# Kernel optimization log

Measured on AMD Instinct MI355X. Metric: run time of the kernel, lower is better.

Reference implementation:

```python
import jax, jax.numpy as jnp
import numpy as np

EPS = 1e-06

def setup_inputs() -> dict:
    key = jax.random.key(0)
    kx, kq, kk, kv = jax.random.split(key, 4)
    B, S, D, F = 8, 4096, 1024, 1024
    # glorot-uniform-ish scale for weights
    scale = (6.0 / (D + F)) ** 0.5
    x = jax.random.normal(kx, (B, S, D), dtype=jnp.float32)
    Wq = jax.random.uniform(kq, (D, F), dtype=jnp.float32, minval=-scale, maxval=scale)
    Wk = jax.random.uniform(kk, (D, F), dtype=jnp.float32, minval=-scale, maxval=scale)
    Wv = jax.random.uniform(kv, (D, F), dtype=jnp.float32, minval=-scale, maxval=scale)
    return {"x": x, "Wq": Wq, "Wk": Wk, "Wv": Wv}


def reference(x, Wq, Wk, Wv):
    # x: [B, S, D]; projections -> [B, S, F]
    queries = jnp.einsum('bsd,df->bsf', x, Wq)
    keys = jnp.einsum('bsd,df->bsf', x, Wk)
    values = jnp.einsum('bsd,df->bsf', x, Wv)
    # feature map: relu(.) + 1 (strictly positive kernel features)
    queries = jax.nn.relu(queries) + 1.0
    keys = jax.nn.relu(keys) + 1.0
    # numerator: K^T V over sequence -> [B, F, F]
    numerator = jnp.einsum('bsf,bsg->bfg', keys, values)
    # denominator: sum of keys over sequence -> [B, 1, F]; broadcasts over last axis
    denominator = jnp.sum(keys, axis=-2, keepdims=True)
    context = numerator / (denominator + EPS)
    # output: context @ Q^T -> [B, F, S]
    output = jnp.einsum('bfg,bsg->bfs', context, queries)
    return output
```

## Files before the change

### kernel.cpp

```cpp
#include <hip/hip_runtime.h>


#define EPSF 1e-6f

constexpr int Bb = 8;
constexpr int Ss = 4096;
constexpr int Dd = 1024;
constexpr int Ff = 1024;

typedef __attribute__((ext_vector_type(8))) short   bf16x8;
typedef __attribute__((ext_vector_type(8))) unsigned short u16x8;
typedef __attribute__((ext_vector_type(4))) float   f32x4;

typedef __attribute__((address_space(3))) unsigned char lds_u8;
typedef __attribute__((address_space(3))) const bf16x8  lds_cvec;

static __device__ __forceinline__ unsigned short f2bf(float f) {
    union { float f; unsigned int u; } v; v.f = f;
    unsigned int r = (v.u + 0x7fffu + ((v.u >> 16) & 1u)) >> 16;
    return (unsigned short)r;
}
static __device__ __forceinline__ float bf2f(unsigned short u) {
    union { unsigned int u; float f; } v; v.u = ((unsigned int)u) << 16;
    return v.f;
}

static __device__ __forceinline__ void gld_lds16(const void* g, lds_u8* l) {
    __builtin_amdgcn_global_load_lds(
        (const __attribute__((address_space(1))) unsigned int*)g,
        (__attribute__((address_space(3))) unsigned int*)l,
        16, 0, 0);
}

__global__ void cvt_x_kernel(const float* __restrict__ x, unsigned short* __restrict__ xb, int n4)
{
    int i = blockIdx.x * blockDim.x + threadIdx.x;
    if (i >= n4) return;
    float4 v = *(const float4*)&x[(size_t)i * 4];
    ushort4 o;
    o.x = f2bf(v.x); o.y = f2bf(v.y); o.z = f2bf(v.z); o.w = f2bf(v.w);
    *(ushort4*)&xb[(size_t)i * 4] = o;
}

__global__ void cvt_wT_kernel(const float* __restrict__ Wq,
                              const float* __restrict__ Wk,
                              const float* __restrict__ Wv,
                              unsigned short* __restrict__ WT)
{
    const int z = blockIdx.z;
    const float* __restrict__ W = (z == 0) ? Wq : (z == 1 ? Wk : Wv);
    unsigned short* __restrict__ dst = WT + (size_t)z * Dd * Ff;

    __shared__ float tile[32][33];
    const int tid = threadIdx.x;
    const int d0 = blockIdx.y * 32, f0 = blockIdx.x * 32;
    const int c = tid & 31, r8 = tid >> 5;
#pragma unroll
    for (int p = 0; p < 4; ++p) {
        int r = p * 8 + r8;
        tile[r][c] = W[(size_t)(d0 + r) * Ff + f0 + c];
    }
    __syncthreads();
#pragma unroll
    for (int p = 0; p < 4; ++p) {
        int r = p * 8 + r8;
        dst[(size_t)(f0 + r) * Dd + d0 + c] = f2bf(tile[c][r]);
    }
}

__global__ void den_kernel(const unsigned short* __restrict__ KbT, float* __restrict__ den)
{
    const int tid = threadIdx.x;
    const int w = tid >> 6, lane = tid & 63;
    const int f = blockIdx.x * 4 + w;
    const int b = blockIdx.y;
    const unsigned short* __restrict__ row = KbT + ((size_t)b * Ff + f) * Ss;
    float s = 0.f;
#pragma unroll
    for (int it = 0; it < Ss / 512; ++it) {
        u16x8 v = *(const u16x8*)&row[it * 512 + lane * 8];
#pragma unroll
        for (int j = 0; j < 8; ++j) s += bf2f(v[j]);
    }
#pragma unroll
    for (int off = 32; off > 0; off >>= 1) s += __shfl_down(s, off, 64);
    if (lane == 0) den[(size_t)b * Ff + f] = s;
}

__global__ void add_ctx_kernel(const unsigned short* __restrict__ p,
                               unsigned short* __restrict__ c)
{
    const int b = blockIdx.y;
    const size_t i8 = ((size_t)blockIdx.x * 256 + threadIdx.x) * 8;
    const u16x8 a0 = *(const u16x8*)(p + (size_t)(2 * b) * Ff * Ff + i8);
    const u16x8 a1 = *(const u16x8*)(p + (size_t)(2 * b + 1) * Ff * Ff + i8);
    u16x8 o;
#pragma unroll
    for (int j = 0; j < 8; ++j) o[j] = f2bf(bf2f(a0[j]) + bf2f(a1[j]));
    *(u16x8*)(c + (size_t)b * Ff * Ff + i8) = o;
}

template<int ACT, int SCALE, int OUT_BF16, int SPLITK2>
__global__ __launch_bounds__(512, 2)
void gemm8(const unsigned short* __restrict__ A,
           const unsigned short* __restrict__ Bt,
           void* __restrict__ Cout,
           const float* __restrict__ den,
           int lda, int ldb, int ldc, int Kdim,
           size_t strideA, size_t strideB, size_t strideC)
{
    __shared__ __align__(16) unsigned char smem_[131072];
    lds_u8* const smem = (lds_u8*)smem_;

    const int gx = gridDim.x, gxy = gx * gridDim.y;
    int flat = blockIdx.z * gxy + blockIdx.y * gx + blockIdx.x;
    const int nwg = gxy * gridDim.z;
    const int cpx = nwg >> 3;
    flat = (flat & 7) * cpx + (flat >> 3);
    const int z = flat / gxy;
    const int rem = flat - z * gxy;
    const int by = rem / gx;
    const int bx = rem - by * gx;

    const int zb   = SPLITK2 ? (z >> 1) : z;
    const int koff = SPLITK2 ? ((z & 1) * Kdim) : 0;

    const unsigned short* __restrict__ Ag  = A  + strideA * zb + koff;
    const unsigned short* __restrict__ Bg  = Bt + strideB * zb + koff;
    const float* __restrict__ denb = SCALE ? (den + (size_t)zb * Ff) : nullptr;

    const int bm = by * 256;
    const int bn = bx * 256;

    const int tid  = threadIdx.x;
    const int wv   = tid >> 6, lane = tid & 63;
    const int wm   = wv >> 2, wn = wv & 3;
    const int lm   = lane & 15;
    const int kg16 = (lane >> 4) << 4;
    const int swz  = (lm & 7) << 4;
    const int kbs  = (((tid & 7) ^ ((tid >> 3) & 7)) << 4);
    const int srow = tid >> 3;

    f32x4 acc[8][4];
#pragma unroll
    for (int i = 0; i < 8; ++i)
#pragma unroll
        for (int j = 0; j < 4; ++j) acc[i][j] = (f32x4){0.f, 0.f, 0.f, 0.f};

    lds_u8* const A0 = smem;
    lds_u8* const B0 = smem + 32768;
    lds_u8* const A1 = smem + 65536;
    lds_u8* const B1 = smem + 98304;

    auto STAGE = [&](int ts, int m, int buf, int h) {
        const unsigned short* gb = m ? Bg : Ag;
        const int ld = m ? ldb : lda;
        const int off0 = m ? bn : bm;
        lds_u8* lb = smem + buf * 65536 + m * 32768 + h * 16384 + wv * 1024;
#pragma unroll
        for (int q = 0; q < 2; ++q) {
            int row = h * 128 + q * 64 + srow;
            const unsigned char* g =
                (const unsigned char*)(gb + (size_t)(off0 + row) * ld + ts * 64) + kbs;
            gld_lds16(g, lb + q * 8192);
        }
    };
    auto LDA4 = [&](bf16x8* dst, int fmb, int kk, lds_u8* Ab) {
#pragma unroll
        for (int f = 0; f < 4; ++f) {
            int r = wm * 128 + (fmb + f) * 16 + lm;
            dst[f] = *(lds_cvec*)(Ab + r * 128 + ((kk * 64 + kg16) ^ swz));
        }
    };
    auto LDB4 = [&](bf16x8* dst, int kk, lds_u8* Bb) {
#pragma unroll
        for (int f = 0; f < 4; ++f) {
            int c = wn * 64 + f * 16 + lm;
            dst[f] = *(lds_cvec*)(Bb + c * 128 + ((kk * 64 + kg16) ^ swz));
        }
    };

#define MM16(a4, b4, mo)                                                        \
    do {                                                                        \
        __builtin_amdgcn_s_setprio(1);                                          \
        _Pragma("unroll")                                                       \
        for (int fm = 0; fm < 4; ++fm)                                          \
            _Pragma("unroll")                                                   \
            for (int fn = 0; fn < 4; ++fn)                                      \
                acc[(mo) + fm][fn] = __builtin_amdgcn_mfma_f32_16x16x32_bf16(   \
                    (b4)[fn], (a4)[fm], acc[(mo) + fm][fn], 0, 0, 0);           \
        __builtin_amdgcn_s_setprio(0);                                          \
    } while (0)

#define FENCE_IN()                                                  \
    do {                                                            \
        __builtin_amdgcn_s_barrier();                               \
        asm volatile("s_waitcnt lgkmcnt(0)");                       \
    } while (0)
#define BAR() __builtin_amdgcn_s_barrier()
#define VM4() asm volatile("s_waitcnt vmcnt(4)")

    const int NT = Kdim >> 6;
    const int NI = NT >> 1;

    STAGE(0, 1, 0, 0); STAGE(0, 1, 0, 1);
    STAGE(0, 0, 0, 0); STAGE(0, 0, 0, 1);
    STAGE(1, 1, 1, 0); STAGE(1, 1, 1, 1);
    VM4();
    BAR();

    for (int i = 0; i < NI; ++i) {
        const int t = 2 * i;
        const int t1s = t + 1;
        const int t2s = (t + 2 < NT) ? t + 2 : NT - 1;
        const int t3s = (t + 3 < NT) ? t + 3 : NT - 1;

        bf16x8 b0r[4], b1r[4], a0r[4], a1r[4];
        LDB4(b0r, 0, B0); LDA4(a0r, 0, 0, A0);
        STAGE(t1s, 0, 1, 0);
        FENCE_IN(); MM16(a0r, b0r, 0); BAR();
        LDA4(a1r, 4, 0, A0); LDB4(b1r, 1, B0);
        STAGE(t1s, 0, 1, 1);
        FENCE_IN(); MM16(a1r, b0r, 4); BAR();
        LDA4(a0r, 0, 1, A0);
        STAGE(t2s, 1, 0, 0);
        FENCE_IN(); MM16(a0r, b1r, 0); BAR();
        LDA4(a1r, 4, 1, A0);
        STAGE(t2s, 1, 0, 1);
        FENCE_IN(); MM16(a1r, b1r, 4); VM4(); BAR();
        LDB4(b0r, 0, B1); LDA4(a0r, 0, 0, A1);
        STAGE(t2s, 0, 0, 0);
        FENCE_IN(); MM16(a0r, b0r, 0); BAR();
        LDA4(a1r, 4, 0, A1); LDB4(b1r, 1, B1);
        STAGE(t2s, 0, 0, 1);
        FENCE_IN(); MM16(a1r, b0r, 4); BAR();
        LDA4(a0r, 0, 1, A1);
        STAGE(t3s, 1, 1, 0);
        FENCE_IN(); MM16(a0r, b1r, 0); BAR();
        LDA4(a1r, 4, 1, A1);
        STAGE(t3s, 1, 1, 1);
        FENCE_IN(); MM16(a1r, b1r, 4); VM4(); BAR();
    }

    asm volatile("s_waitcnt vmcnt(0)");

    const int hi4 = (lane >> 4) * 4;
#pragma unroll
    for (int fm = 0; fm < 8; ++fm) {
        const int gr = bm + wm * 128 + fm * 16 + lm;
#pragma unroll
        for (int fn = 0; fn < 4; ++fn) {
            const int gcn = bn + wn * 64 + fn * 16 + hi4;
            f32x4 v = acc[fm][fn];
            if (ACT) {
#pragma unroll
                for (int e = 0; e < 4; ++e) v[e] = fmaxf(v[e], 0.f) + 1.f;
            }
            if (SCALE) {
                float4 d4 = *(const float4*)&denb[gcn];
                v[0] *= 1.f / (d4.x + EPSF);
                v[1] *= 1.f / (d4.y + EPSF);
                v[2] *= 1.f / (d4.z + EPSF);
                v[3] *= 1.f / (d4.w + EPSF);
            }
            if (OUT_BF16) {
                ushort4 o;
                o.x = f2bf(v[0]); o.y = f2bf(v[1]); o.z = f2bf(v[2]); o.w = f2bf(v[3]);
                *(ushort4*)((unsigned short*)Cout + strideC * z + (size_t)gr * ldc + gcn) = o;
            } else {
                *(float4*)((float*)Cout + strideC * z + (size_t)gr * ldc + gcn) =
                    *(float4*)&v;
            }
        }
    }
#undef MM16
#undef FENCE_IN
#undef BAR
#undef VM4
}

extern "C" void kernel_launch(void* const* d_in, const int* in_sizes, int n_in,
                              void* d_out, int out_size, void* d_ws, size_t ws_size,
                              hipStream_t stream)
{
    (void)in_sizes; (void)n_in; (void)out_size;
    const float* x  = (const float*)d_in[0];
    const float* Wq = (const float*)d_in[1];
    const float* Wk = (const float*)d_in[2];
    const float* Wv = (const float*)d_in[3];
    float* out = (float*)d_out;

    const size_t nx   = (size_t)Bb * Ss * Dd;
    const size_t nW   = (size_t)3 * Dd * Ff;
    const size_t nQKV = (size_t)Bb * Ss * Ff;
    const size_t nCtx = (size_t)Bb * Ff * Ff;
    const size_t nP   = (size_t)16 * Ff * Ff;

    unsigned short* xb   = (unsigned short*)d_ws;
    unsigned short* WT   = xb + nx;
    unsigned short* Qb   = WT + nW;
    unsigned short* KbT  = Qb + nQKV;
    unsigned short* VbT  = KbT + nQKV;
    unsigned short* ctxb = VbT + nQKV;
    float* den = (float*)(ctxb + nCtx);
    unsigned short* pctx = (unsigned short*)(den + (size_t)Bb * Ff);

    const size_t need_split =
        ((nx + nW + 3 * nQKV + nCtx + nP) * 2 + (size_t)Bb * Ff * 4);
    const bool do_split = ws_size >= need_split;

    cvt_x_kernel<<<dim3((int)(nx / 4 / 256)), 256, 0, stream>>>(x, xb, (int)(nx / 4));
    cvt_wT_kernel<<<dim3(Ff / 32, Dd / 32, 3), 256, 0, stream>>>(Wq, Wk, Wv, WT);

    gemm8<1, 0, 1, 0><<<dim3(Ss / 256, Ff / 256, Bb), 512, 0, stream>>>(
        WT + (size_t)1 * Dd * Ff, xb, KbT, nullptr,
        Dd, Dd, Ss, Dd, 0, (size_t)Ss * Dd, (size_t)Ff * Ss);

    den_kernel<<<dim3(Ff / 4, Bb), 256, 0, stream>>>(KbT, den);

    gemm8<1, 1, 1, 0><<<dim3(Ff / 256, Ss / 256, Bb), 512, 0, stream>>>(
        xb, WT + (size_t)0 * Dd * Ff, Qb, den,
        Dd, Dd, Ff, Dd, (size_t)Ss * Dd, 0, (size_t)Ss * Ff);

    gemm8<0, 0, 1, 0><<<dim3(Ss / 256, Ff / 256, Bb), 512, 0, stream>>>(
        WT + (size_t)2 * Dd * Ff, xb, VbT, nullptr,
        Dd, Dd, Ss, Dd, 0, (size_t)Ss * Dd, (size_t)Ff * Ss);

    if (do_split) {
        gemm8<0, 0, 1, 1><<<dim3(Ff / 256, Ff / 256, 2 * Bb), 512, 0, stream>>>(
            KbT, VbT, pctx, nullptr,
            Ss, Ss, Ff, Ss / 2, (size_t)Ff * Ss, (size_t)Ff * Ss, (size_t)Ff * Ff);
        add_ctx_kernel<<<dim3(Ff * Ff / 8 / 256, Bb), 256, 0, stream>>>(pctx, ctxb);
    } else {
        gemm8<0, 0, 1, 0><<<dim3(Ff / 256, Ff / 256, Bb), 512, 0, stream>>>(
            KbT, VbT, ctxb, nullptr,
            Ss, Ss, Ff, Ss, (size_t)Ff * Ss, (size_t)Ff * Ss, (size_t)Ff * Ff);
    }

    gemm8<0, 0, 0, 0><<<dim3(Ss / 256, Ff / 256, Bb), 512, 0, stream>>>(
        ctxb, Qb, out, nullptr,
        Ff, Ff, Ss, Ff, (size_t)Ff * Ff, (size_t)Ss * Ff, (size_t)Ff * Ss);
}
```

Baseline: 414.0 us.

## Software-pipeline LDS fragment loads one phase ahead of MFMA in GEMM loop

```diff
diff --git a/kernel.cpp b/kernel.cpp
--- a/kernel.cpp
+++ b/kernel.cpp
@@ -192,13 +192,18 @@
         __builtin_amdgcn_s_setprio(0);                                          \
     } while (0)
 
-#define FENCE_IN()                                                  \
+#define PHEND()                                                     \
     do {                                                            \
+        asm volatile("s_waitcnt lgkmcnt(0)");                       \
+        __builtin_amdgcn_sched_barrier(0);                          \
         __builtin_amdgcn_s_barrier();                               \
-        asm volatile("s_waitcnt lgkmcnt(0)");                       \
     } while (0)
-#define BAR() __builtin_amdgcn_s_barrier()
-#define VM4() asm volatile("s_waitcnt vmcnt(4)")
+#define PHEND_VM2()                                                 \
+    do {                                                            \
+        asm volatile("s_waitcnt vmcnt(2) lgkmcnt(0)");              \
+        __builtin_amdgcn_sched_barrier(0);                          \
+        __builtin_amdgcn_s_barrier();                               \
+    } while (0)
 
     const int NT = Kdim >> 6;
     const int NI = NT >> 1;
@@ -206,8 +211,11 @@
     STAGE(0, 1, 0, 0); STAGE(0, 1, 0, 1);
     STAGE(0, 0, 0, 0); STAGE(0, 0, 0, 1);
     STAGE(1, 1, 1, 0); STAGE(1, 1, 1, 1);
-    VM4();
-    BAR();
+    asm volatile("s_waitcnt vmcnt(4)");
+    __builtin_amdgcn_s_barrier();
+
+    bf16x8 a03[4], a47[4], b0[4], b1[4];
+    LDB4(b0, 0, B0); LDA4(a03, 0, 0, A0);
 
     for (int i = 0; i < NI; ++i) {
         const int t = 2 * i;
@@ -215,31 +223,38 @@
         const int t2s = (t + 2 < NT) ? t + 2 : NT - 1;
         const int t3s = (t + 3 < NT) ? t + 3 : NT - 1;
 
-        bf16x8 b0r[4], b1r[4], a0r[4], a1r[4];
-        LDB4(b0r, 0, B0); LDA4(a0r, 0, 0, A0);
         STAGE(t1s, 0, 1, 0);
-        FENCE_IN(); MM16(a0r, b0r, 0); BAR();
-        LDA4(a1r, 4, 0, A0); LDB4(b1r, 1, B0);
+        LDA4(a47, 4, 0, A0);
+        MM16(a03, b0, 0);
+        PHEND();
         STAGE(t1s, 0, 1, 1);
-        FENCE_IN(); MM16(a1r, b0r, 4); BAR();
-        LDA4(a0r, 0, 1, A0);
+        LDA4(a03, 0, 1, A0); LDB4(b1, 1, B0);
+        MM16(a47, b0, 4);
+        PHEND();
         STAGE(t2s, 1, 0, 0);
-        FENCE_IN(); MM16(a0r, b1r, 0); BAR();
-        LDA4(a1r, 4, 1, A0);
+        LDA4(a47, 4, 1, A0);
+        MM16(a03, b1, 0);
+        PHEND_VM2();
         STAGE(t2s, 1, 0, 1);
-        FENCE_IN(); MM16(a1r, b1r, 4); VM4(); BAR();
-        LDB4(b0r, 0, B1); LDA4(a0r, 0, 0, A1);
+        LDA4(a03, 0, 0, A1); LDB4(b0, 0, B1);
+        MM16(a47, b1, 4);
+        PHEND();
         STAGE(t2s, 0, 0, 0);
-        FENCE_IN(); MM16(a0r, b0r, 0); BAR();
-        LDA4(a1r, 4, 0, A1); LDB4(b1r, 1, B1);
+        LDA4(a47, 4, 0, A1);
+        MM16(a03, b0, 0);
+        PHEND();
         STAGE(t2s, 0, 0, 1);
-        FENCE_IN(); MM16(a1r, b0r, 4); BAR();
-        LDA4(a0r, 0, 1, A1);
+        LDA4(a03, 0, 1, A1); LDB4(b1, 1, B1);
+        MM16(a47, b0, 4);
+        PHEND();
         STAGE(t3s, 1, 1, 0);
-        FENCE_IN(); MM16(a0r, b1r, 0); BAR();
-        LDA4(a1r, 4, 1, A1);
+        LDA4(a47, 4, 1, A1);
+        MM16(a03, b1, 0);
+        PHEND_VM2();
         STAGE(t3s, 1, 1, 1);
-        FENCE_IN(); MM16(a1r, b1r, 4); VM4(); BAR();
+        LDA4(a03, 0, 0, A0); LDB4(b0, 0, B0);
+        MM16(a47, b1, 4);
+        PHEND();
     }
 
     asm volatile("s_waitcnt vmcnt(0)");
@@ -274,9 +289,8 @@
         }
     }
 #undef MM16
-#undef FENCE_IN
-#undef BAR
-#undef VM4
+#undef PHEND
+#undef PHEND_VM2
 }
 
 extern "C" void kernel_launch(void* const* d_in, const int* in_sizes, int n_in,
```

After: 412.7 us. About the same (-0.3%).

## Shrink GEMM tiles to 128x128 with 4 waves and simple double-buffered loop

Applied to the files above, without the earlier changes.

```diff
diff --git a/kernel.cpp b/kernel.cpp
--- a/kernel.cpp
+++ b/kernel.cpp
@@ -101,7 +101,7 @@
 }
 
 template<int ACT, int SCALE, int OUT_BF16, int SPLITK2>
-__global__ __launch_bounds__(512, 2)
+__global__ __launch_bounds__(256, 2)
 void gemm8(const unsigned short* __restrict__ A,
            const unsigned short* __restrict__ Bt,
            void* __restrict__ Cout,
@@ -109,7 +109,7 @@
            int lda, int ldb, int ldc, int Kdim,
            size_t strideA, size_t strideB, size_t strideC)
 {
-    __shared__ __align__(16) unsigned char smem_[131072];
+    __shared__ __align__(16) unsigned char smem_[65536];
     lds_u8* const smem = (lds_u8*)smem_;
 
     const int gx = gridDim.x, gxy = gx * gridDim.y;
@@ -129,125 +129,93 @@
     const unsigned short* __restrict__ Bg  = Bt + strideB * zb + koff;
     const float* __restrict__ denb = SCALE ? (den + (size_t)zb * Ff) : nullptr;
 
-    const int bm = by * 256;
-    const int bn = bx * 256;
+    const int bm = by * 128;
+    const int bn = bx * 128;
 
     const int tid  = threadIdx.x;
     const int wv   = tid >> 6, lane = tid & 63;
-    const int wm   = wv >> 2, wn = wv & 3;
+    const int wm   = wv >> 1, wn = wv & 1;
     const int lm   = lane & 15;
     const int kg16 = (lane >> 4) << 4;
     const int swz  = (lm & 7) << 4;
     const int kbs  = (((tid & 7) ^ ((tid >> 3) & 7)) << 4);
     const int srow = tid >> 3;
 
-    f32x4 acc[8][4];
-#pragma unroll
-    for (int i = 0; i < 8; ++i)
+    f32x4 acc[4][4];
+#pragma unroll
+    for (int i = 0; i < 4; ++i)
 #pragma unroll
         for (int j = 0; j < 4; ++j) acc[i][j] = (f32x4){0.f, 0.f, 0.f, 0.f};
 
-    lds_u8* const A0 = smem;
-    lds_u8* const B0 = smem + 32768;
-    lds_u8* const A1 = smem + 65536;
-    lds_u8* const B1 = smem + 98304;
-
-    auto STAGE = [&](int ts, int m, int buf, int h) {
+    auto STAGE = [&](int ts, int m, int buf) {
         const unsigned short* gb = m ? Bg : Ag;
         const int ld = m ? ldb : lda;
         const int off0 = m ? bn : bm;
-        lds_u8* lb = smem + buf * 65536 + m * 32768 + h * 16384 + wv * 1024;
-#pragma unroll
-        for (int q = 0; q < 2; ++q) {
-            int row = h * 128 + q * 64 + srow;
+        lds_u8* lb = smem + buf * 32768 + m * 16384 + wv * 1024;
+#pragma unroll
+        for (int q = 0; q < 4; ++q) {
+            int row = q * 32 + srow;
             const unsigned char* g =
                 (const unsigned char*)(gb + (size_t)(off0 + row) * ld + ts * 64) + kbs;
-            gld_lds16(g, lb + q * 8192);
+            gld_lds16(g, lb + q * 4096);
         }
     };
-    auto LDA4 = [&](bf16x8* dst, int fmb, int kk, lds_u8* Ab) {
+    auto LD4 = [&](bf16x8* dst, int kk, lds_u8* base, int w0) {
 #pragma unroll
         for (int f = 0; f < 4; ++f) {
-            int r = wm * 128 + (fmb + f) * 16 + lm;
-            dst[f] = *(lds_cvec*)(Ab + r * 128 + ((kk * 64 + kg16) ^ swz));
+            int r = w0 * 64 + f * 16 + lm;
+            dst[f] = *(lds_cvec*)(base + r * 128 + ((kk * 64 + kg16) ^ swz));
         }
     };
-    auto LDB4 = [&](bf16x8* dst, int kk, lds_u8* Bb) {
-#pragma unroll
-        for (int f = 0; f < 4; ++f) {
-            int c = wn * 64 + f * 16 + lm;
-            dst[f] = *(lds_cvec*)(Bb + c * 128 + ((kk * 64 + kg16) ^ swz));
-        }
-    };
-
-#define MM16(a4, b4, mo)                                                        \
+
+#define MM16(a4, b4)                                                            \
     do {                                                                        \
         __builtin_amdgcn_s_setprio(1);                                          \
         _Pragma("unroll")                                                       \
         for (int fm = 0; fm < 4; ++fm)                                          \
             _Pragma("unroll")                                                   \
             for (int fn = 0; fn < 4; ++fn)                                      \
-                acc[(mo) + fm][fn] = __builtin_amdgcn_mfma_f32_16x16x32_bf16(   \
-                    (b4)[fn], (a4)[fm], acc[(mo) + fm][fn], 0, 0, 0);           \
+                acc[fm][fn] = __builtin_amdgcn_mfma_f32_16x16x32_bf16(          \
+                    (b4)[fn], (a4)[fm], acc[fm][fn], 0, 0, 0);                  \
         __builtin_amdgcn_s_setprio(0);                                          \
     } while (0)
 
-#define FENCE_IN()                                                  \
+#define LGKM0_FENCE()                                               \
     do {                                                            \
-        __builtin_amdgcn_s_barrier();                               \
         asm volatile("s_waitcnt lgkmcnt(0)");                       \
+        __builtin_amdgcn_sched_barrier(0);                          \
     } while (0)
-#define BAR() __builtin_amdgcn_s_barrier()
-#define VM4() asm volatile("s_waitcnt vmcnt(4)")
 
     const int NT = Kdim >> 6;
-    const int NI = NT >> 1;
-
-    STAGE(0, 1, 0, 0); STAGE(0, 1, 0, 1);
-    STAGE(0, 0, 0, 0); STAGE(0, 0, 0, 1);
-    STAGE(1, 1, 1, 0); STAGE(1, 1, 1, 1);
-    VM4();
-    BAR();
-
-    for (int i = 0; i < NI; ++i) {
-        const int t = 2 * i;
-        const int t1s = t + 1;
-        const int t2s = (t + 2 < NT) ? t + 2 : NT - 1;
-        const int t3s = (t + 3 < NT) ? t + 3 : NT - 1;
-
-        bf16x8 b0r[4], b1r[4], a0r[4], a1r[4];
-        LDB4(b0r, 0, B0); LDA4(a0r, 0, 0, A0);
-        STAGE(t1s, 0, 1, 0);
-        FENCE_IN(); MM16(a0r, b0r, 0); BAR();
-        LDA4(a1r, 4, 0, A0); LDB4(b1r, 1, B0);
-        STAGE(t1s, 0, 1, 1);
-        FENCE_IN(); MM16(a1r, b0r, 4); BAR();
-        LDA4(a0r, 0, 1, A0);
-        STAGE(t2s, 1, 0, 0);
-        FENCE_IN(); MM16(a0r, b1r, 0); BAR();
-        LDA4(a1r, 4, 1, A0);
-        STAGE(t2s, 1, 0, 1);
-        FENCE_IN(); MM16(a1r, b1r, 4); VM4(); BAR();
-        LDB4(b0r, 0, B1); LDA4(a0r, 0, 0, A1);
-        STAGE(t2s, 0, 0, 0);
-        FENCE_IN(); MM16(a0r, b0r, 0); BAR();
-        LDA4(a1r, 4, 0, A1); LDB4(b1r, 1, B1);
-        STAGE(t2s, 0, 0, 1);
-        FENCE_IN(); MM16(a1r, b0r, 4); BAR();
-        LDA4(a0r, 0, 1, A1);
-        STAGE(t3s, 1, 1, 0);
-        FENCE_IN(); MM16(a0r, b1r, 0); BAR();
-        LDA4(a1r, 4, 1, A1);
-        STAGE(t3s, 1, 1, 1);
-        FENCE_IN(); MM16(a1r, b1r, 4); VM4(); BAR();
-    }
-
+
+    STAGE(0, 0, 0); STAGE(0, 1, 0);
     asm volatile("s_waitcnt vmcnt(0)");
+    __builtin_amdgcn_s_barrier();
+
+    for (int t = 0; t < NT; ++t) {
+        const int buf = t & 1;
+        lds_u8* Ab  = smem + buf * 32768;
+        lds_u8* Bbs = Ab + 16384;
+        if (t + 1 < NT) {
+            STAGE(t + 1, 0, buf ^ 1);
+            STAGE(t + 1, 1, buf ^ 1);
+        }
+        bf16x8 a0[4], b0r[4], a1[4], b1r[4];
+        LD4(a0, 0, Ab, wm); LD4(b0r, 0, Bbs, wn);
+        LGKM0_FENCE();
+        MM16(a0, b0r);
+        LD4(a1, 1, Ab, wm); LD4(b1r, 1, Bbs, wn);
+        LGKM0_FENCE();
+        MM16(a1, b1r);
+        asm volatile("s_waitcnt vmcnt(0)");
+        __builtin_amdgcn_sched_barrier(0);
+        __builtin_amdgcn_s_barrier();
+    }
 
     const int hi4 = (lane >> 4) * 4;
 #pragma unroll
-    for (int fm = 0; fm < 8; ++fm) {
-        const int gr = bm + wm * 128 + fm * 16 + lm;
+    for (int fm = 0; fm < 4; ++fm) {
+        const int gr = bm + wm * 64 + fm * 16 + lm;
 #pragma unroll
         for (int fn = 0; fn < 4; ++fn) {
             const int gcn = bn + wn * 64 + fn * 16 + hi4;
@@ -274,9 +242,7 @@
         }
     }
 #undef MM16
-#undef FENCE_IN
-#undef BAR
-#undef VM4
+#undef LGKM0_FENCE
 }
 
 extern "C" void kernel_launch(void* const* d_in, const int* in_sizes, int n_in,
@@ -312,32 +278,32 @@
     cvt_x_kernel<<<dim3((int)(nx / 4 / 256)), 256, 0, stream>>>(x, xb, (int)(nx / 4));
     cvt_wT_kernel<<<dim3(Ff / 32, Dd / 32, 3), 256, 0, stream>>>(Wq, Wk, Wv, WT);
 
-    gemm8<1, 0, 1, 0><<<dim3(Ss / 256, Ff / 256, Bb), 512, 0, stream>>>(
+    gemm8<1, 0, 1, 0><<<dim3(Ss / 128, Ff / 128, Bb), 256, 0, stream>>>(
         WT + (size_t)1 * Dd * Ff, xb, KbT, nullptr,
         Dd, Dd, Ss, Dd, 0, (size_t)Ss * Dd, (size_t)Ff * Ss);
 
     den_kernel<<<dim3(Ff / 4, Bb), 256, 0, stream>>>(KbT, den);
 
-    gemm8<1, 1, 1, 0><<<dim3(Ff / 256, Ss / 256, Bb), 512, 0, stream>>>(
+    gemm8<1, 1, 1, 0><<<dim3(Ff / 128, Ss / 128, Bb), 256, 0, stream>>>(
         xb, WT + (size_t)0 * Dd * Ff, Qb, den,
         Dd, Dd, Ff, Dd, (size_t)Ss * Dd, 0, (size_t)Ss * Ff);
 
-    gemm8<0, 0, 1, 0><<<dim3(Ss / 256, Ff / 256, Bb), 512, 0, stream>>>(
+    gemm8<0, 0, 1, 0><<<dim3(Ss / 128, Ff / 128, Bb), 256, 0, stream>>>(
         WT + (size_t)2 * Dd * Ff, xb, VbT, nullptr,
         Dd, Dd, Ss, Dd, 0, (size_t)Ss * Dd, (size_t)Ff * Ss);
 
     if (do_split) {
-        gemm8<0, 0, 1, 1><<<dim3(Ff / 256, Ff / 256, 2 * Bb), 512, 0, stream>>>(
+        gemm8<0, 0, 1, 1><<<dim3(Ff / 128, Ff / 128, 2 * Bb), 256, 0, stream>>>(
             KbT, VbT, pctx, nullptr,
             Ss, Ss, Ff, Ss / 2, (size_t)Ff * Ss, (size_t)Ff * Ss, (size_t)Ff * Ff);
         add_ctx_kernel<<<dim3(Ff * Ff / 8 / 256, Bb), 256, 0, stream>>>(pctx, ctxb);
     } else {
-        gemm8<0, 0, 1, 0><<<dim3(Ff / 256, Ff / 256, Bb), 512, 0, stream>>>(
+        gemm8<0, 0, 1, 0><<<dim3(Ff / 128, Ff / 128, Bb), 256, 0, stream>>>(
             KbT, VbT, ctxb, nullptr,
             Ss, Ss, Ff, Ss, (size_t)Ff * Ss, (size_t)Ff * Ss, (size_t)Ff * Ff);
     }
 
-    gemm8<0, 0, 0, 0><<<dim3(Ss / 256, Ff / 256, Bb), 512, 0, stream>>>(
+    gemm8<0, 0, 0, 0><<<dim3(Ss / 128, Ff / 128, Bb), 256, 0, stream>>>(
         ctxb, Qb, out, nullptr,
         Ff, Ff, Ss, Ff, (size_t)Ff * Ff, (size_t)Ss * Ff, (size_t)Ff * Ss);
 }
```

Result: slower. 480.5 us (+16.0%).
